# Performance work log

Hardware: AMD Instinct MI355X
Metric: run time of the kernel (lower is better)

The kernel has to match this reference:

```python
import jax, jax.numpy as jnp
import numpy as np
from functools import partial

NX, NY = 48, 48
LX, LY = 1.0, 1.0
T, DT = 0.01, 0.0001
NT = int(T / DT)  # 100 sequential explicit-Euler steps
DX, DY = LX / NX, LY / NY
TWO_PI = 2.0 * jnp.pi


def setup_inputs() -> dict:
    key = jax.random.key(0)
    u0 = jax.random.normal(key, (8192, 1, NX, NY), dtype=jnp.float32)
    return {
        "u0": u0,
        "alpha_w1": jnp.float32(0.1),
        "alpha_w2": jnp.float32(0.1),
        "alpha_w3": jnp.float32(0.1),
        "beta_w1": jnp.float32(0.3),
        "beta_w2": jnp.float32(0.2),
        "beta_w3": jnp.float32(0.1),
    }


def _coeff_grids(a1, a2, a3, b1, b2, b3):
    x = jnp.linspace(0.0, LX, NX)
    y = jnp.linspace(0.0, LY, NY)
    yy, xx = jnp.meshgrid(y, x, indexing="ij")  # (NY, NX), matches torch.meshgrid(y, x, 'ij')
    alpha = 0.5 * DT * (jnp.abs(a1) + jnp.abs(a2) * jnp.sin(TWO_PI * yy)
                        + jnp.abs(a3) * jnp.cos(TWO_PI * yy)) / DX ** 2
    beta = DT * (jnp.abs(b1) + jnp.abs(b2) * jnp.cos(TWO_PI * xx)
                 + jnp.abs(b3) * jnp.sin(TWO_PI * xx)) / DY ** 2
    return alpha[None], beta[None]  # (1, NY, NX) broadcast over batch (square grid)


def reference(u0, alpha_w1, alpha_w2, alpha_w3, beta_w1, beta_w2, beta_w3):
    alpha_grid, beta_grid = _coeff_grids(alpha_w1, alpha_w2, alpha_w3,
                                         beta_w1, beta_w2, beta_w3)
    u = u0[:, 0]  # (B, NX, NY)
    # reflect-pad once; the boundary ring stays frozen across all timesteps
    u = jnp.pad(u, ((0, 0), (1, 1), (1, 1)), mode="reflect")

    def step(u, _):
        ui = u[:, 1:-1, 1:-1]
        u_xx = u[:, 2:, 1:-1] - 2.0 * ui + u[:, :-2, 1:-1]
        u_yy = u[:, 1:-1, 2:] - 2.0 * ui + u[:, 1:-1, :-2]
        u = u.at[:, 1:-1, 1:-1].set(ui + alpha_grid * u_xx + beta_grid * u_yy)
        return u, None

    u, _ = jax.lax.scan(step, u, None, length=NT)
    return u[:, 1:-1, 1:-1][:, None]  # (B, 1, NX, NY)
```

## Files before the change

### kernel.cpp

```cpp
#include <hip/hip_runtime.h>
#include <hip/hip_fp16.h>
#include <math.h>


#define NTSTEPS 100

typedef __half2 h2;

__device__ __forceinline__ h2 dpp_row_shr1(h2 oldv, h2 x) {
    int r = __builtin_amdgcn_update_dpp(
        __builtin_bit_cast(int, oldv), __builtin_bit_cast(int, x),
        0x111, 0xF, 0xF, false);
    return __builtin_bit_cast(h2, r);
}
__device__ __forceinline__ h2 dpp_row_shl1(h2 oldv, h2 x) {
    int r = __builtin_amdgcn_update_dpp(
        __builtin_bit_cast(int, oldv), __builtin_bit_cast(int, x),
        0x101, 0xF, 0xF, false);
    return __builtin_bit_cast(h2, r);
}
__device__ __forceinline__ h2 bperm(int addr, h2 x) {
    int r = __builtin_amdgcn_ds_bpermute(addr, __builtin_bit_cast(int, x));
    return __builtin_bit_cast(h2, r);
}

__global__ void coeff_kernel(
    const float* __restrict__ pa1, const float* __restrict__ pa2,
    const float* __restrict__ pa3, const float* __restrict__ pb1,
    const float* __restrict__ pb2, const float* __restrict__ pb3,
    float* __restrict__ ws)
{
    int tid = threadIdx.x;
    if (tid < 48) {
        float a1 = fabsf(pa1[0]), a2 = fabsf(pa2[0]), a3 = fabsf(pa3[0]);
        float b1 = fabsf(pb1[0]), b2 = fabsf(pb2[0]), b3 = fabsf(pb3[0]);
        float t = 6.283185307179586f * ((float)tid / 47.0f);
        float s = sinf(t), c = cosf(t);
        ws[tid]      = 0.1152f * (a1 + a2 * s + a3 * c);
        ws[48 + tid] = 0.2304f * (b1 + b2 * c + b3 * s);
    }
}

__global__ __launch_bounds__(256) void pde_kernel(
    const float* __restrict__ u0,
    const float* __restrict__ cw,
    float* __restrict__ out)
{
    const int tid  = threadIdx.x;
    const int lane = tid & 63;
    const int wv   = tid >> 6;
    const int pair = blockIdx.x * 4 + wv;
    const int tx   = lane & 15;
    const int ty   = lane >> 4;
    const int c0   = 3 * tx;
    const int r0   = 12 * ty;

    const float* __restrict__ srcA = u0 + (size_t)(2 * pair) * 2304;
    const float* __restrict__ srcB = srcA + 2304;

    h2 a[12], b[3];
    #pragma unroll
    for (int k = 0; k < 12; ++k) a[k] = __half2half2(__float2half(cw[r0 + k]));
    #pragma unroll
    for (int c = 0; c < 3; ++c) b[c] = __half2half2(__float2half(cw[48 + c0 + c]));
    const h2 neg2 = __floats2half2_rn(-2.0f, -2.0f);

    h2 u[12][3];
    h2 ep[12];
    h2 tH[3], bH[3];

    const int epc = (tx == 15) ? 46 : 1;
    #pragma unroll
    for (int k = 0; k < 12; ++k) {
        #pragma unroll
        for (int c = 0; c < 3; ++c) {
            int o = (r0 + k) * 48 + c0 + c;
            u[k][c] = __floats2half2_rn(srcA[o], srcB[o]);
        }
        int oe = (r0 + k) * 48 + epc;
        ep[k] = __floats2half2_rn(srcA[oe], srcB[oe]);
    }
    {
        const int tor = (ty == 0) ? 1 : (r0 - 1);
        const int bor = (ty == 3) ? 46 : (r0 + 12);
        #pragma unroll
        for (int c = 0; c < 3; ++c) {
            int ot = tor * 48 + c0 + c, ob = bor * 48 + c0 + c;
            tH[c] = __floats2half2_rn(srcA[ot], srcB[ot]);
            bH[c] = __floats2half2_rn(srcA[ob], srcB[ob]);
        }
    }

    const int upA = ((lane - 16) & 63) << 2;
    const int dnA = ((lane + 16) & 63) << 2;
    const bool notTop = (ty != 0);
    const bool notBot = (ty != 3);

    #pragma unroll 1
    for (int t = 0; t < NTSTEPS; ++t) {
        #pragma unroll
        for (int c = 0; c < 3; ++c) {
            h2 tv = bperm(upA, u[11][c]);
            h2 bv = bperm(dnA, u[0][c]);
            tH[c] = notTop ? tv : tH[c];
            bH[c] = notBot ? bv : bH[c];
        }
        h2 p0 = tH[0], p1 = tH[1], p2 = tH[2];
        #pragma unroll
        for (int k = 0; k < 12; ++k) {
            const h2 x0 = u[k][0], x1 = u[k][1], x2 = u[k][2];
            const h2 hl = dpp_row_shr1(ep[k], x2);
            const h2 hr = dpp_row_shl1(ep[k], x0);
            const h2 d0 = (k == 11) ? bH[0] : u[k + 1][0];
            const h2 d1 = (k == 11) ? bH[1] : u[k + 1][1];
            const h2 d2 = (k == 11) ? bH[2] : u[k + 1][2];
            const h2 s10 = __hadd2(p0, d0);
            const h2 s11 = __hadd2(p1, d1);
            const h2 s12 = __hadd2(p2, d2);
            const h2 s20 = __hadd2(hl, x1);
            const h2 s21 = __hadd2(x0, x2);
            const h2 s22 = __hadd2(x1, hr);
            const h2 t10 = __hfma2(neg2, x0, s10);
            const h2 t11 = __hfma2(neg2, x1, s11);
            const h2 t12 = __hfma2(neg2, x2, s12);
            const h2 t20 = __hfma2(neg2, x0, s20);
            const h2 t21 = __hfma2(neg2, x1, s21);
            const h2 t22 = __hfma2(neg2, x2, s22);
            const h2 n0 = __hfma2(b[0], t20, __hfma2(a[k], t10, x0));
            const h2 n1 = __hfma2(b[1], t21, __hfma2(a[k], t11, x1));
            const h2 n2 = __hfma2(b[2], t22, __hfma2(a[k], t12, x2));
            p0 = x0; p1 = x1; p2 = x2;
            u[k][0] = n0; u[k][1] = n1; u[k][2] = n2;
        }
    }

    float* __restrict__ dstA = out + (size_t)(2 * pair) * 2304;
    float* __restrict__ dstB = dstA + 2304;
    #pragma unroll
    for (int k = 0; k < 12; ++k) {
        #pragma unroll
        for (int c = 0; c < 3; ++c) {
            int o = (r0 + k) * 48 + c0 + c;
            dstA[o] = __low2float(u[k][c]);
            dstB[o] = __high2float(u[k][c]);
        }
    }
}

extern "C" void kernel_launch(void* const* d_in, const int* in_sizes, int n_in,
                              void* d_out, int out_size, void* d_ws, size_t ws_size,
                              hipStream_t stream) {
    const float* u0 = (const float*)d_in[0];
    float* ws = (float*)d_ws;
    coeff_kernel<<<1, 64, 0, stream>>>(
        (const float*)d_in[1], (const float*)d_in[2], (const float*)d_in[3],
        (const float*)d_in[4], (const float*)d_in[5], (const float*)d_in[6],
        ws);
    pde_kernel<<<1024, 256, 0, stream>>>(u0, ws, (float*)d_out);
}
```

Before: 335.7 us.

## Replace time-stepping with separable eigen-decomposition propagator applied in closed form

Replaces the 100-step explicit stencil loop with a spectral solution. Small kernels compute eigenvectors of the separable 1D operators (bisection plus inverse iteration and Gram-Schmidt) and tabulate per-mode growth factors G=(1+λ)^100 and geometric sums for the frozen boundary forcing. The main kernel then applies four 48x48 matrix multiplies per image in fp32, plus boundary-forcing corrections. This removes the long sequential loop and the fp16 arithmetic, but depends on the fp32 accuracy of the eigensolver, including for non-symmetric reflect boundaries.

```diff
diff --git a/kernel.cpp b/kernel.cpp
--- a/kernel.cpp
+++ b/kernel.cpp
@@ -1,150 +1,331 @@
 #include <hip/hip_runtime.h>
-#include <hip/hip_fp16.h>
 #include <math.h>
 
 
-#define NTSTEPS 100
-
-typedef __half2 h2;
-
-__device__ __forceinline__ h2 dpp_row_shr1(h2 oldv, h2 x) {
-    int r = __builtin_amdgcn_update_dpp(
-        __builtin_bit_cast(int, oldv), __builtin_bit_cast(int, x),
-        0x111, 0xF, 0xF, false);
-    return __builtin_bit_cast(h2, r);
-}
-__device__ __forceinline__ h2 dpp_row_shl1(h2 oldv, h2 x) {
-    int r = __builtin_amdgcn_update_dpp(
-        __builtin_bit_cast(int, oldv), __builtin_bit_cast(int, x),
-        0x101, 0xF, 0xF, false);
-    return __builtin_bit_cast(h2, r);
-}
-__device__ __forceinline__ h2 bperm(int addr, h2 x) {
-    int r = __builtin_amdgcn_ds_bpermute(addr, __builtin_bit_cast(int, x));
-    return __builtin_bit_cast(h2, r);
-}
-
-__global__ void coeff_kernel(
+#define WS_LAM   0
+#define WS_QC0   96
+#define WS_QC47  144
+#define WS_QTAB  288
+#define WS_PTAB  4896
+#define WS_G     9504
+#define WS_S     11808
+
+__global__ __launch_bounds__(64) void eig_kernel(
     const float* __restrict__ pa1, const float* __restrict__ pa2,
     const float* __restrict__ pa3, const float* __restrict__ pb1,
     const float* __restrict__ pb2, const float* __restrict__ pb3,
     float* __restrict__ ws)
 {
-    int tid = threadIdx.x;
-    if (tid < 48) {
-        float a1 = fabsf(pa1[0]), a2 = fabsf(pa2[0]), a3 = fabsf(pa3[0]);
-        float b1 = fabsf(pb1[0]), b2 = fabsf(pb2[0]), b3 = fabsf(pb3[0]);
-        float t = 6.283185307179586f * ((float)tid / 47.0f);
+    __shared__ float sc[48], sd[48], se[48], smu[48];
+    __shared__ float sred[2];
+    __shared__ float fD[48][49], fDL[48][49], fU1[48][49], fU2[48][49];
+    __shared__ float sx[48][49], sv[48][49];
+    __shared__ unsigned char fP[48][48];
+
+    const int which = blockIdx.x;
+    const int l = threadIdx.x;
+
+    if (l < 48) {
+        float t = 6.283185307179586f * ((float)l / 47.0f);
         float s = sinf(t), c = cosf(t);
-        ws[tid]      = 0.1152f * (a1 + a2 * s + a3 * c);
-        ws[48 + tid] = 0.2304f * (b1 + b2 * c + b3 * s);
+        sc[l] = (which == 0)
+            ? 0.1152f * (fabsf(pa1[0]) + fabsf(pa2[0]) * s + fabsf(pa3[0]) * c)
+            : 0.2304f * (fabsf(pb1[0]) + fabsf(pb2[0]) * c + fabsf(pb3[0]) * s);
+    }
+    __syncthreads();
+
+    if (l < 48) {
+        float a2 = (float)(l + 2) / (float)(l + 1);
+        float d = a2 * sc[l];
+        if (l < 47) {
+            float b2 = (float)(l + 1) / (float)(l + 2);
+            d += b2 * sc[l + 1];
+            se[l] = -sqrtf(b2) * sc[l + 1] * sqrtf((float)(l + 3) / (float)(l + 2));
+        } else se[l] = 0.f;
+        sd[l] = d;
+    }
+    __syncthreads();
+
+    if (l == 0) {
+        float lo = 1e30f, hi = -1e30f;
+        for (int i = 0; i < 48; ++i) {
+            float em = (i > 0) ? fabsf(se[i - 1]) : 0.f;
+            float ep = (i < 47) ? fabsf(se[i]) : 0.f;
+            lo = fminf(lo, sd[i] - em - ep);
+            hi = fmaxf(hi, sd[i] + em + ep);
+        }
+        sred[0] = lo - 1e-6f; sred[1] = hi + 1e-6f;
+    }
+    __syncthreads();
+
+    float mu = 0.f;
+    if (l < 48) {
+        float lo = sred[0], hi = sred[1];
+        for (int it = 0; it < 48; ++it) {
+            float x = 0.5f * (lo + hi);
+            int cnt = 0; float q = 1.0f;
+            for (int i = 0; i < 48; ++i) {
+                float e2 = (i > 0) ? se[i - 1] * se[i - 1] : 0.f;
+                q = sd[i] - x - e2 / q;
+                if (fabsf(q) < 1e-30f) q = -1e-30f;
+                cnt += (q < 0.f) ? 1 : 0;
+            }
+            if (cnt <= l) lo = x; else hi = x;
+        }
+        mu = 0.5f * (lo + hi);
+        smu[l] = mu;
+        ws[WS_LAM + 48 * which + l] = -mu;
+    }
+    __syncthreads();
+
+    if (l < 48) {
+        for (int i = 0; i < 48; ++i) {
+            fD[i][l]  = sd[i] - mu;
+            fDL[i][l] = (i > 0)  ? se[i - 1] : 0.f;
+            fU1[i][l] = (i < 47) ? se[i] : 0.f;
+            fU2[i][l] = 0.f;
+            fP[i][l]  = 0;
+        }
+        for (int i = 0; i < 47; ++i) {
+            float di = fD[i][l], sub = fDL[i + 1][l];
+            if (fabsf(di) >= fabsf(sub)) {
+                float fact = (di != 0.f) ? sub / di : 0.f;
+                fDL[i + 1][l] = fact;
+                fD[i + 1][l] -= fact * fU1[i][l];
+            } else {
+                float fact = di / sub;
+                fD[i][l] = sub; fDL[i + 1][l] = fact;
+                float tmp = fU1[i][l];
+                fU1[i][l] = fD[i + 1][l];
+                fD[i + 1][l] = tmp - fact * fD[i + 1][l];
+                if (i < 46) { fU2[i][l] = fU1[i + 1][l]; fU1[i + 1][l] = -fact * fU1[i + 1][l]; }
+                fP[i][l] = 1;
+            }
+        }
+        for (int i = 0; i < 48; ++i) {
+            float d = fD[i][l];
+            if (fabsf(d) < 1e-12f) fD[i][l] = (d >= 0.f) ? 1e-12f : -1e-12f;
+        }
+        for (int i = 0; i < 48; ++i) {
+            unsigned h = (unsigned)(i * 1664525u) + (unsigned)((l + 1) * 1013904223u);
+            h ^= h >> 16; h *= 2654435761u; h ^= h >> 13;
+            sx[i][l] = (float)(h & 0xFFFF) * (1.0f / 65536.0f) - 0.5f;
+        }
+        for (int pass = 0; pass < 3; ++pass) {
+            for (int i = 0; i < 47; ++i) {
+                if (!fP[i][l]) {
+                    sx[i + 1][l] -= fDL[i + 1][l] * sx[i][l];
+                } else {
+                    float t1 = sx[i][l];
+                    sx[i][l] = sx[i + 1][l];
+                    sx[i + 1][l] = t1 - fDL[i + 1][l] * sx[i + 1][l];
+                }
+            }
+            sx[47][l] /= fD[47][l];
+            sx[46][l] = (sx[46][l] - fU1[46][l] * sx[47][l]) / fD[46][l];
+            for (int i = 45; i >= 0; --i)
+                sx[i][l] = (sx[i][l] - fU1[i][l] * sx[i + 1][l] - fU2[i][l] * sx[i + 2][l]) / fD[i][l];
+            float nrm = 0.f;
+            for (int i = 0; i < 48; ++i) nrm += sx[i][l] * sx[i][l];
+            float inv = 1.0f / sqrtf(fmaxf(nrm, 1e-30f));
+            for (int i = 0; i < 48; ++i) sx[i][l] *= inv;
+        }
+    }
+    __syncthreads();
+
+    for (int j = 0; j < 48; ++j) {
+        if (l > j && l < 48) {
+            float dot = 0.f;
+            for (int i = 0; i < 48; ++i) dot += sx[i][j] * sx[i][l];
+            for (int i = 0; i < 48; ++i) sx[i][l] -= dot * sx[i][j];
+        }
+        __syncthreads();
+        if (l == j + 1 && l < 48) {
+            float nrm = 0.f;
+            for (int i = 0; i < 48; ++i) nrm += sx[i][l] * sx[i][l];
+            float inv = 1.0f / sqrtf(fmaxf(nrm, 1e-30f));
+            for (int i = 0; i < 48; ++i) sx[i][l] *= inv;
+        }
+        __syncthreads();
+    }
+
+    if (l < 48) {
+        sv[47][l] = sx[47][l] / sqrtf(49.0f / 48.0f);
+        for (int i = 46; i >= 0; --i) {
+            float ai = sqrtf((float)(i + 2) / (float)(i + 1));
+            float bi = -sqrtf((float)(i + 1) / (float)(i + 2));
+            sv[i][l] = (sx[i][l] - bi * sv[i + 1][l]) / ai;
+        }
+    }
+    __syncthreads();
+
+    if (l < 48) {
+        for (int i = 0; i < 48; ++i)
+            ws[WS_PTAB + 2304 * which + l * 48 + i] = sv[i][l];
+        for (int k = 0; k < 48; ++k) {
+            float ak = sqrtf((float)(k + 2) / (float)(k + 1));
+            float v = ak * sx[k][l];
+            if (k > 0) v -= sqrtf((float)k / (float)(k + 1)) * sx[k - 1][l];
+            ws[WS_QTAB + 2304 * which + k * 48 + l] = v;
+        }
+        float a0  = sqrtf(2.0f);
+        float a47 = sqrtf(49.0f / 48.0f);
+        float b46 = -sqrtf(47.0f / 48.0f);
+        ws[WS_QC0  + 96 * which + l] = sc[0]  * (a0 * sx[0][l]);
+        ws[WS_QC47 + 96 * which + l] = sc[47] * (a47 * sx[47][l] + b46 * sx[46][l]);
     }
 }
 
-__global__ __launch_bounds__(256) void pde_kernel(
-    const float* __restrict__ u0,
-    const float* __restrict__ cw,
+__global__ __launch_bounds__(256) void gs_kernel(float* __restrict__ ws)
+{
+    int idx = blockIdx.x * 256 + threadIdx.x;
+    if (idx >= 2304) return;
+    int p = idx / 48, q = idx % 48;
+    float d = ws[p] + ws[48 + q];
+    float r = 1.0f + d;
+    float r2 = r * r, r4 = r2 * r2, r8 = r4 * r4;
+    float r16 = r8 * r8, r32 = r16 * r16, r64 = r32 * r32;
+    float G = r64 * r32 * r4;
+    float S;
+    if (fabsf(d) > 1e-3f) S = (G - 1.0f) / d;
+    else S = 100.f + d * (4950.f + d * 161700.f);
+    ws[WS_G + idx] = G;
+    ws[WS_S + idx] = S;
+}
+
+__global__ __launch_bounds__(256, 2) void prop_kernel(
+    const float* __restrict__ u0, const float* __restrict__ ws,
     float* __restrict__ out)
 {
-    const int tid  = threadIdx.x;
-    const int lane = tid & 63;
-    const int wv   = tid >> 6;
-    const int pair = blockIdx.x * 4 + wv;
-    const int tx   = lane & 15;
-    const int ty   = lane >> 4;
-    const int c0   = 3 * tx;
-    const int r0   = 12 * ty;
-
-    const float* __restrict__ srcA = u0 + (size_t)(2 * pair) * 2304;
-    const float* __restrict__ srcB = srcA + 2304;
-
-    h2 a[12], b[3];
-    #pragma unroll
-    for (int k = 0; k < 12; ++k) a[k] = __half2half2(__float2half(cw[r0 + k]));
-    #pragma unroll
-    for (int c = 0; c < 3; ++c) b[c] = __half2half2(__float2half(cw[48 + c0 + c]));
-    const h2 neg2 = __floats2half2_rn(-2.0f, -2.0f);
-
-    h2 u[12][3];
-    h2 ep[12];
-    h2 tH[3], bH[3];
-
-    const int epc = (tx == 15) ? 46 : 1;
-    #pragma unroll
-    for (int k = 0; k < 12; ++k) {
-        #pragma unroll
-        for (int c = 0; c < 3; ++c) {
-            int o = (r0 + k) * 48 + c0 + c;
-            u[k][c] = __floats2half2_rn(srcA[o], srcB[o]);
-        }
-        int oe = (r0 + k) * 48 + epc;
-        ep[k] = __floats2half2_rn(srcA[oe], srcB[oe]);
-    }
-    {
-        const int tor = (ty == 0) ? 1 : (r0 - 1);
-        const int bor = (ty == 3) ? 46 : (r0 + 12);
-        #pragma unroll
-        for (int c = 0; c < 3; ++c) {
-            int ot = tor * 48 + c0 + c, ob = bor * 48 + c0 + c;
-            tH[c] = __floats2half2_rn(srcA[ot], srcB[ot]);
-            bH[c] = __floats2half2_rn(srcA[ob], srcB[ob]);
-        }
-    }
-
-    const int upA = ((lane - 16) & 63) << 2;
-    const int dnA = ((lane + 16) & 63) << 2;
-    const bool notTop = (ty != 0);
-    const bool notBot = (ty != 3);
-
-    #pragma unroll 1
-    for (int t = 0; t < NTSTEPS; ++t) {
-        #pragma unroll
-        for (int c = 0; c < 3; ++c) {
-            h2 tv = bperm(upA, u[11][c]);
-            h2 bv = bperm(dnA, u[0][c]);
-            tH[c] = notTop ? tv : tH[c];
-            bH[c] = notBot ? bv : bH[c];
-        }
-        h2 p0 = tH[0], p1 = tH[1], p2 = tH[2];
-        #pragma unroll
-        for (int k = 0; k < 12; ++k) {
-            const h2 x0 = u[k][0], x1 = u[k][1], x2 = u[k][2];
-            const h2 hl = dpp_row_shr1(ep[k], x2);
-            const h2 hr = dpp_row_shl1(ep[k], x0);
-            const h2 d0 = (k == 11) ? bH[0] : u[k + 1][0];
-            const h2 d1 = (k == 11) ? bH[1] : u[k + 1][1];
-            const h2 d2 = (k == 11) ? bH[2] : u[k + 1][2];
-            const h2 s10 = __hadd2(p0, d0);
-            const h2 s11 = __hadd2(p1, d1);
-            const h2 s12 = __hadd2(p2, d2);
-            const h2 s20 = __hadd2(hl, x1);
-            const h2 s21 = __hadd2(x0, x2);
-            const h2 s22 = __hadd2(x1, hr);
-            const h2 t10 = __hfma2(neg2, x0, s10);
-            const h2 t11 = __hfma2(neg2, x1, s11);
-            const h2 t12 = __hfma2(neg2, x2, s12);
-            const h2 t20 = __hfma2(neg2, x0, s20);
-            const h2 t21 = __hfma2(neg2, x1, s21);
-            const h2 t22 = __hfma2(neg2, x2, s22);
-            const h2 n0 = __hfma2(b[0], t20, __hfma2(a[k], t10, x0));
-            const h2 n1 = __hfma2(b[1], t21, __hfma2(a[k], t11, x1));
-            const h2 n2 = __hfma2(b[2], t22, __hfma2(a[k], t12, x2));
-            p0 = x0; p1 = x1; p2 = x2;
-            u[k][0] = n0; u[k][1] = n1; u[k][2] = n2;
-        }
-    }
-
-    float* __restrict__ dstA = out + (size_t)(2 * pair) * 2304;
-    float* __restrict__ dstB = dstA + 2304;
-    #pragma unroll
-    for (int k = 0; k < 12; ++k) {
-        #pragma unroll
-        for (int c = 0; c < 3; ++c) {
-            int o = (r0 + k) * 48 + c0 + c;
-            dstA[o] = __low2float(u[k][c]);
-            dstB[o] = __high2float(u[k][c]);
-        }
-    }
+    __shared__ float scr[4][2304];
+    __shared__ float vecs[4][4][48];
+
+    const int tid = threadIdx.x, lane = tid & 63, w = tid >> 6;
+    const int img = blockIdx.x * 4 + w;
+    const int rq = lane & 15, cq = lane >> 4;
+    const int p0 = 3 * rq, q0 = 12 * cq;
+    const float* __restrict__ src = u0 + (size_t)img * 2304;
+    float* __restrict__ dst = out + (size_t)img * 2304;
+    const float* __restrict__ QLT = ws + WS_QTAB;
+    const float* __restrict__ QR  = ws + WS_QTAB + 2304;
+    const float* __restrict__ PLT = ws + WS_PTAB;
+    const float* __restrict__ PR  = ws + WS_PTAB + 2304;
+    const float* __restrict__ Gt  = ws + WS_G;
+    const float* __restrict__ St  = ws + WS_S;
+
+    float C[3][12], D[3][12];
+
+    #pragma unroll
+    for (int r = 0; r < 3; ++r)
+        #pragma unroll
+        for (int c = 0; c < 12; ++c) C[r][c] = 0.f;
+    #pragma unroll 4
+    for (int k = 0; k < 48; ++k) {
+        float a0 = QLT[k * 48 + p0], a1 = QLT[k * 48 + p0 + 1], a2 = QLT[k * 48 + p0 + 2];
+        float b[12];
+        #pragma unroll
+        for (int c = 0; c < 12; ++c) b[c] = src[k * 48 + q0 + c];
+        #pragma unroll
+        for (int c = 0; c < 12; ++c) {
+            C[0][c] = fmaf(a0, b[c], C[0][c]);
+            C[1][c] = fmaf(a1, b[c], C[1][c]);
+            C[2][c] = fmaf(a2, b[c], C[2][c]);
+        }
+    }
+    #pragma unroll
+    for (int r = 0; r < 3; ++r)
+        #pragma unroll
+        for (int c = 0; c < 12; ++c) scr[w][(q0 + c) * 48 + p0 + r] = C[r][c];
+    if (lane < 48) {
+        float wt = 0.f, wb = 0.f, vl = 0.f, vr = 0.f;
+        #pragma unroll 4
+        for (int j = 0; j < 48; ++j) {
+            float ptj = src[48 + j], pbj = src[46 * 48 + j];
+            float plj = src[j * 48 + 1], prj = src[j * 48 + 46];
+            float qr = QR[j * 48 + lane], ql = QLT[j * 48 + lane];
+            wt = fmaf(qr, ptj, wt); wb = fmaf(qr, pbj, wb);
+            vl = fmaf(ql, plj, vl); vr = fmaf(ql, prj, vr);
+        }
+        vecs[w][0][lane] = wt; vecs[w][1][lane] = wb;
+        vecs[w][2][lane] = vl; vecs[w][3][lane] = vr;
+    }
+    __syncthreads();
+    #pragma unroll
+    for (int r = 0; r < 3; ++r)
+        #pragma unroll
+        for (int c = 0; c < 12; ++c) D[r][c] = 0.f;
+    #pragma unroll 4
+    for (int j = 0; j < 48; ++j) {
+        float a0 = scr[w][j * 48 + p0], a1 = scr[w][j * 48 + p0 + 1], a2 = scr[w][j * 48 + p0 + 2];
+        float b[12];
+        #pragma unroll
+        for (int c = 0; c < 12; ++c) b[c] = QR[j * 48 + q0 + c];
+        #pragma unroll
+        for (int c = 0; c < 12; ++c) {
+            D[0][c] = fmaf(a0, b[c], D[0][c]);
+            D[1][c] = fmaf(a1, b[c], D[1][c]);
+            D[2][c] = fmaf(a2, b[c], D[2][c]);
+        }
+    }
+    __syncthreads();
+    #pragma unroll
+    for (int r = 0; r < 3; ++r) {
+        int p = p0 + r;
+        float qc0v = ws[WS_QC0 + p], qc47v = ws[WS_QC47 + p];
+        float vlp = vecs[w][2][p], vrp = vecs[w][3][p];
+        #pragma unroll
+        for (int c = 0; c < 12; ++c) {
+            int q = q0 + c;
+            float ch = qc0v * vecs[w][0][q] + qc47v * vecs[w][1][q]
+                     + vlp * ws[WS_QC0 + 96 + q] + vrp * ws[WS_QC47 + 96 + q];
+            scr[w][p * 48 + q] = Gt[p * 48 + q] * D[r][c] + St[p * 48 + q] * ch;
+        }
+    }
+    __syncthreads();
+    #pragma unroll
+    for (int r = 0; r < 3; ++r)
+        #pragma unroll
+        for (int c = 0; c < 12; ++c) C[r][c] = 0.f;
+    #pragma unroll 4
+    for (int k = 0; k < 48; ++k) {
+        float a0 = PLT[k * 48 + p0], a1 = PLT[k * 48 + p0 + 1], a2 = PLT[k * 48 + p0 + 2];
+        float b[12];
+        #pragma unroll
+        for (int c = 0; c < 12; ++c) b[c] = scr[w][k * 48 + q0 + c];
+        #pragma unroll
+        for (int c = 0; c < 12; ++c) {
+            C[0][c] = fmaf(a0, b[c], C[0][c]);
+            C[1][c] = fmaf(a1, b[c], C[1][c]);
+            C[2][c] = fmaf(a2, b[c], C[2][c]);
+        }
+    }
+    __syncthreads();
+    #pragma unroll
+    for (int r = 0; r < 3; ++r)
+        #pragma unroll
+        for (int c = 0; c < 12; ++c) scr[w][(q0 + c) * 48 + p0 + r] = C[r][c];
+    __syncthreads();
+    #pragma unroll
+    for (int r = 0; r < 3; ++r)
+        #pragma unroll
+        for (int c = 0; c < 12; ++c) D[r][c] = 0.f;
+    #pragma unroll 4
+    for (int q = 0; q < 48; ++q) {
+        float a0 = scr[w][q * 48 + p0], a1 = scr[w][q * 48 + p0 + 1], a2 = scr[w][q * 48 + p0 + 2];
+        float b[12];
+        #pragma unroll
+        for (int c = 0; c < 12; ++c) b[c] = PR[q * 48 + q0 + c];
+        #pragma unroll
+        for (int c = 0; c < 12; ++c) {
+            D[0][c] = fmaf(a0, b[c], D[0][c]);
+            D[1][c] = fmaf(a1, b[c], D[1][c]);
+            D[2][c] = fmaf(a2, b[c], D[2][c]);
+        }
+    }
+    #pragma unroll
+    for (int r = 0; r < 3; ++r)
+        #pragma unroll
+        for (int c = 0; c < 12; ++c) dst[(p0 + r) * 48 + q0 + c] = D[r][c];
 }
 
 extern "C" void kernel_launch(void* const* d_in, const int* in_sizes, int n_in,
@@ -152,9 +333,9 @@
                               hipStream_t stream) {
     const float* u0 = (const float*)d_in[0];
     float* ws = (float*)d_ws;
-    coeff_kernel<<<1, 64, 0, stream>>>(
+    eig_kernel<<<2, 64, 0, stream>>>(
         (const float*)d_in[1], (const float*)d_in[2], (const float*)d_in[3],
-        (const float*)d_in[4], (const float*)d_in[5], (const float*)d_in[6],
-        ws);
-    pde_kernel<<<1024, 256, 0, stream>>>(u0, ws, (float*)d_out);
+        (const float*)d_in[4], (const float*)d_in[5], (const float*)d_in[6], ws);
+    gs_kernel<<<9, 256, 0, stream>>>(ws);
+    prop_kernel<<<2048, 256, 0, stream>>>(u0, ws, (float*)d_out);
 }
```

Measured after the change: 640.0 us. +90.6%, slower.
